# Performance work log

Hardware: AMD Instinct MI355X
Metric: run time of the kernel (lower is better)

The kernel has to match this reference:

```python
import jax, jax.numpy as jnp
import numpy as np

B, T, C, UNITS = 64, 1000, 320, 320


def _lstm_scan(x_tbc, m_tb, W, U, b):
    """Masked LSTM over leading time axis.
    x_tbc: [T,B,C], m_tb: [T,B] bool. Keras gate order i,f,c(g),o.
    Masked steps carry (h,c) through unchanged and emit the carried h,
    matching Keras masking semantics. Returns (ys [T,B,U], h_T [B,U]).
    """
    units = U.shape[0]
    h0 = jnp.zeros((x_tbc.shape[1], units), x_tbc.dtype)

    def step(carry, inp):
        h, c = carry
        xt, mt = inp
        z = xt @ W + h @ U + b                      # [B, 4U]
        i, f, g, o = jnp.split(z, 4, axis=-1)
        i = jax.nn.sigmoid(i)
        f = jax.nn.sigmoid(f)
        g = jnp.tanh(g)
        o = jax.nn.sigmoid(o)
        c_new = f * c + i * g
        h_new = o * jnp.tanh(c_new)
        mt = mt[:, None]
        h = jnp.where(mt, h_new, h)
        c = jnp.where(mt, c_new, c)
        return (h, c), h

    (hT, cT), ys = jax.lax.scan(step, (h0, h0), (x_tbc, m_tb))
    return ys, hT


def setup_inputs() -> dict:
    key = jax.random.key(0)
    ks = jax.random.split(key, 8)
    inputs = jax.random.normal(ks[0], (B, T, C), dtype=jnp.float32)
    # padding mask: variable sequence lengths in [T//2, T]
    seq_len = jax.random.randint(ks[1], (B,), T // 2, T + 1)
    mask = (jnp.arange(T)[None, :] < seq_len[:, None])  # [B, T] bool
    s_in = 1.0 / np.sqrt(C)
    s_rec = 1.0 / np.sqrt(UNITS)
    W_fwd = jax.random.normal(ks[2], (C, 4 * UNITS), jnp.float32) * s_in
    U_fwd = jax.random.normal(ks[3], (UNITS, 4 * UNITS), jnp.float32) * s_rec
    b_fwd = jnp.zeros((4 * UNITS,), jnp.float32).at[UNITS:2 * UNITS].set(1.0)  # unit forget bias
    W_bwd = jax.random.normal(ks[4], (C, 4 * UNITS), jnp.float32) * s_in
    U_bwd = jax.random.normal(ks[5], (UNITS, 4 * UNITS), jnp.float32) * s_rec
    b_bwd = jnp.zeros((4 * UNITS,), jnp.float32).at[UNITS:2 * UNITS].set(1.0)
    return {"inputs": inputs, "mask": mask, "W_fwd": W_fwd, "U_fwd": U_fwd,
            "b_fwd": b_fwd, "W_bwd": W_bwd, "U_bwd": U_bwd, "b_bwd": b_bwd}


def reference(inputs, mask, W_fwd, U_fwd, b_fwd, W_bwd, U_bwd, b_bwd):
    x = jnp.transpose(inputs, (1, 0, 2))   # [T,B,C]
    m = jnp.transpose(mask, (1, 0))        # [T,B]
    # forward direction
    ys_f, h_f = _lstm_scan(x, m, W_fwd, U_fwd, b_fwd)
    # backward direction: go_backwards reverses time; Bidirectional flips output back
    ys_b, h_b = _lstm_scan(x[::-1], m[::-1], W_bwd, U_bwd, b_bwd)
    ys_b = ys_b[::-1]
    sequence_output = jnp.transpose(jnp.concatenate([ys_f, ys_b], axis=-1), (1, 0, 2))  # [B,T,2U]
    state_output = jnp.concatenate([h_f, h_b], axis=-1)  # [B,2U]
    return sequence_output, state_output
```

## Files before the change

### kernel.cpp

```cpp
#include <hip/hip_runtime.h>
#include <hip/hip_bf16.h>
#include <stdint.h>


#define Bx 64
#define Tx 1000
#define Cx 320
#define NSLICE 20
#define UPW 16

typedef __attribute__((ext_vector_type(8))) short short8;
typedef __attribute__((ext_vector_type(4))) short short4v;
typedef __attribute__((ext_vector_type(4))) float f32x4;

__device__ inline unsigned short f2bf(float f) {
  unsigned x = __builtin_bit_cast(unsigned, f);
  x += 0x7fffu + ((x >> 16) & 1u);
  return (unsigned short)(x >> 16);
}
__device__ inline float bf2f(unsigned short u) {
  unsigned x = ((unsigned)u) << 16;
  return __builtin_bit_cast(float, x);
}

#define OFF_MB   0ull
#define OFF_BAR  8192ull
#define OFF_HB   16384ull
#define OFF_XB   0ull
#define OFF_WT   40960000ull
#define OFF_BP   42598400ull
#define OFF_ZX   42608640ull

__global__ __launch_bounds__(256) void k_prep_x(const float* __restrict__ X,
                                                unsigned short* __restrict__ Xb) {
  int i4 = blockIdx.x * 256 + threadIdx.x;
  if (i4 >= Bx * Tx * Cx / 4) return;
  int idx = i4 * 4;
  int b = idx / (Tx * Cx);
  int rem = idx - b * (Tx * Cx);
  int t = rem / Cx;
  int c = rem - t * Cx;
  float4 v = *(const float4*)(X + idx);
  short4v o;
  o[0] = (short)f2bf(v.x); o[1] = (short)f2bf(v.y);
  o[2] = (short)f2bf(v.z); o[3] = (short)f2bf(v.w);
  *(short4v*)(Xb + (size_t)(t * Bx + b) * Cx + c) = o;
}

__global__ __launch_bounds__(256) void k_prep_w(const float* __restrict__ Wf,
                                                const float* __restrict__ Wb,
                                                const float* __restrict__ bfv,
                                                const float* __restrict__ bbv,
                                                unsigned short* __restrict__ Wt,
                                                float* __restrict__ biasp) {
  int gid = blockIdx.x * 256 + threadIdx.x;
  if (gid < 2 * 1280 * 320) {
    int dir = gid / (1280 * 320);
    int rem = gid - dir * 1280 * 320;
    int n = rem / 320;
    int k = rem - n * 320;
    int u = n >> 2, g = n & 3;
    const float* W = dir ? Wb : Wf;
    Wt[gid] = f2bf(W[k * 1280 + g * 320 + u]);
  }
  if (gid < 2 * 1280) {
    int dir = gid / 1280, n = gid - dir * 1280;
    int u = n >> 2, g = n & 3;
    const float* bsrc = dir ? bbv : bfv;
    biasp[gid] = bsrc[g * 320 + u];
  }
}

__global__ __launch_bounds__(256) void k_prep_mask(const void* __restrict__ maskp,
                                                   unsigned long long* __restrict__ mask2) {
  int t = blockIdx.x * 256 + threadIdx.x;
  if (t >= Tx) return;
  const unsigned* mw = (const unsigned*)maskp;
  const bool mbyte = (mw[0] == 0x01010101u);
  unsigned long long wv = 0ull;
  if (mbyte) {
    const unsigned char* m8 = (const unsigned char*)maskp;
#pragma unroll 8
    for (int b = 0; b < Bx; b++)
      wv |= (unsigned long long)(m8[b * Tx + t] & 1) << b;
  } else {
    const int* m32 = (const int*)maskp;
#pragma unroll 8
    for (int b = 0; b < Bx; b++)
      wv |= (unsigned long long)(m32[b * Tx + t] & 1) << b;
  }
  mask2[t] = wv;
}

__global__ __launch_bounds__(256) void k_gemm(const unsigned short* __restrict__ A,
                                              const unsigned short* __restrict__ Bt,
                                              const float* __restrict__ biasp,
                                              unsigned short* __restrict__ Czx) {
  int bid = blockIdx.x;
  int dir = bid / 5000;
  int r = bid - dir * 5000;
  int tm = r / 10, tn = r - (r / 10) * 10;
  long m0 = (long)tm * 128;
  int n0 = tn * 128;
  const unsigned short* Bd = Bt + (size_t)dir * 1280 * 320;
  const float* bias = biasp + dir * 1280;

  __shared__ __align__(16) unsigned short As[128 * 64];
  __shared__ __align__(16) unsigned short Bs[128 * 64];

  int tid = threadIdx.x;
  int wave = tid >> 6, lane = tid & 63;
  int l15 = lane & 15, l4 = lane >> 4;

  f32x4 acc[2][8];
#pragma unroll
  for (int i = 0; i < 2; i++)
#pragma unroll
    for (int j = 0; j < 8; j++) acc[i][j] = (f32x4){0.f, 0.f, 0.f, 0.f};

  for (int k0 = 0; k0 < 320; k0 += 64) {
    __syncthreads();
#pragma unroll
    for (int it = 0; it < 4; it++) {
      int idx = it * 256 + tid;
      int rr = idx >> 3, cc = idx & 7;
      const unsigned short* ga = A + (size_t)(m0 + rr) * 320 + k0 + cc * 8;
      unsigned short* la = As + (size_t)(it * 256 + wave * 64) * 8;
      __builtin_amdgcn_global_load_lds(
          (const __attribute__((address_space(1))) void*)ga,
          (__attribute__((address_space(3))) void*)la, 16, 0, 0);
      const unsigned short* gb = Bd + (size_t)(n0 + rr) * 320 + k0 + cc * 8;
      unsigned short* lb = Bs + (size_t)(it * 256 + wave * 64) * 8;
      __builtin_amdgcn_global_load_lds(
          (const __attribute__((address_space(1))) void*)gb,
          (__attribute__((address_space(3))) void*)lb, 16, 0, 0);
    }
    __syncthreads();
#pragma unroll
    for (int kk = 0; kk < 2; kk++) {
      short8 af[2], bf8[8];
#pragma unroll
      for (int mf = 0; mf < 2; mf++)
        af[mf] = *(const short8*)(As + (wave * 32 + mf * 16 + l15) * 64 + kk * 32 + l4 * 8);
#pragma unroll
      for (int nf = 0; nf < 8; nf++)
        bf8[nf] = *(const short8*)(Bs + (nf * 16 + l15) * 64 + kk * 32 + l4 * 8);
#pragma unroll
      for (int mf = 0; mf < 2; mf++)
#pragma unroll
        for (int nf = 0; nf < 8; nf++)
          acc[mf][nf] = __builtin_amdgcn_mfma_f32_16x16x32_bf16(af[mf], bf8[nf], acc[mf][nf], 0, 0, 0);
    }
  }
#pragma unroll
  for (int mf = 0; mf < 2; mf++) {
#pragma unroll
    for (int nf = 0; nf < 8; nf++) {
      int col = n0 + nf * 16 + l15;
      float bv = bias[col];
      int slice = col >> 6, i64v = col & 63;
      size_t sbase = ((size_t)(dir * NSLICE + slice)) * Tx * 4096;
#pragma unroll
      for (int i = 0; i < 4; i++) {
        long m = m0 + wave * 32 + mf * 16 + l4 * 4 + i;
        long t = m >> 6;
        int b = (int)(m & 63);
        Czx[sbase + (size_t)t * 4096 + b * 64 + i64v] = f2bf(acc[mf][nf][i] + bv);
      }
    }
  }
}

__global__ __launch_bounds__(256, 1) void k_lstm(const unsigned short* __restrict__ Zx,
                                                 const float* __restrict__ Uf,
                                                 const float* __restrict__ Ub,
                                                 const unsigned long long* __restrict__ mask2,
                                                 unsigned short* __restrict__ hbuf,
                                                 float* __restrict__ out,
                                                 unsigned* __restrict__ bar) {
  const int w = blockIdx.x;
  const int dir = w / NSLICE;
  const int slice = w - dir * NSLICE;
  const int u0 = slice * UPW;
  const int tid = threadIdx.x;
  const int wave = tid >> 6, lane = tid & 63;
  const int l15 = lane & 15, l4 = lane >> 4;

  const float* U = dir ? Ub : Uf;
  short8 bfrag[4][10];
#pragma unroll
  for (int nf = 0; nf < 4; nf++) {
    int ncol = nf * 16 + l15;
    int colU = (ncol & 3) * 320 + u0 + (ncol >> 2);
#pragma unroll
    for (int kt = 0; kt < 10; kt++) {
      short8 v;
#pragma unroll
      for (int j = 0; j < 8; j++)
        v[j] = (short)f2bf(U[(size_t)(kt * 32 + l4 * 8 + j) * 1280 + colU]);
      bfrag[nf][kt] = v;
    }
  }

  const int pb = tid >> 2;
  const int uq = tid & 3;
  const int arow = wave * 16 + l15;
  float c0 = 0.f, c1 = 0.f, c2 = 0.f, c3 = 0.f;
  float h0 = 0.f, h1 = 0.f, h2 = 0.f, h3 = 0.f;

  __shared__ float zsh[64][68];

  unsigned* slots = bar + dir * NSLICE * 16;
  const unsigned short* zbase = Zx + ((size_t)(dir * NSLICE + slice)) * Tx * 4096;

  int t = dir ? (Tx - 1) : 0;
  short8 zv0 = *(const short8*)(zbase + (size_t)t * 4096 + pb * 64 + uq * 16);
  short8 zv1 = *(const short8*)(zbase + (size_t)t * 4096 + pb * 64 + uq * 16 + 8);
  unsigned long long mwrd = mask2[t];

  for (int s = 0;; ++s) {
    t = dir ? (Tx - 1 - s) : s;
    float4 zr0, zr1, zr2, zr3;
    if (s > 0) {
      if (tid < NSLICE) {
        while (__hip_atomic_load(&slots[tid * 16], __ATOMIC_RELAXED,
                                 __HIP_MEMORY_SCOPE_AGENT) < (unsigned)s)
          __builtin_amdgcn_s_sleep(1);
      }
      __syncthreads();

      const unsigned short* hr = hbuf + ((size_t)((s & 1) * 2 + dir)) * Bx * 320;
      const unsigned short* hp = hr + arow * 320 + l4 * 8;
      short8 afr[10];
#pragma unroll
      for (int kt = 0; kt < 10; kt++) {
        union { unsigned long long q[2]; short8 v; } u;
        u.q[0] = __hip_atomic_load((const unsigned long long*)(hp + kt * 32),
                                   __ATOMIC_RELAXED, __HIP_MEMORY_SCOPE_AGENT);
        u.q[1] = __hip_atomic_load((const unsigned long long*)(hp + kt * 32 + 4),
                                   __ATOMIC_RELAXED, __HIP_MEMORY_SCOPE_AGENT);
        afr[kt] = u.v;
      }
#pragma unroll
      for (int nf = 0; nf < 4; nf++) {
        f32x4 a0 = {0.f, 0.f, 0.f, 0.f}, a1 = {0.f, 0.f, 0.f, 0.f};
#pragma unroll
        for (int k2 = 0; k2 < 5; k2++) {
          a0 = __builtin_amdgcn_mfma_f32_16x16x32_bf16(afr[2 * k2], bfrag[nf][2 * k2], a0, 0, 0, 0);
          a1 = __builtin_amdgcn_mfma_f32_16x16x32_bf16(afr[2 * k2 + 1], bfrag[nf][2 * k2 + 1], a1, 0, 0, 0);
        }
        int rr = wave * 16 + l4 * 4;
        zsh[rr + 0][nf * 16 + l15] = a0[0] + a1[0];
        zsh[rr + 1][nf * 16 + l15] = a0[1] + a1[1];
        zsh[rr + 2][nf * 16 + l15] = a0[2] + a1[2];
        zsh[rr + 3][nf * 16 + l15] = a0[3] + a1[3];
      }
      __syncthreads();
      zr0 = *(const float4*)&zsh[pb][uq * 16 + 0];
      zr1 = *(const float4*)&zsh[pb][uq * 16 + 4];
      zr2 = *(const float4*)&zsh[pb][uq * 16 + 8];
      zr3 = *(const float4*)&zsh[pb][uq * 16 + 12];
    } else {
      zr0 = zr1 = zr2 = zr3 = make_float4(0.f, 0.f, 0.f, 0.f);
    }

    int mv = (int)((mwrd >> pb) & 1ull);
#define GATES(CC, HH, Z0, Z1, Z2, Z3, ZR)                              \
    {                                                                  \
      float zi = bf2f((unsigned short)(Z0)) + (ZR).x;                  \
      float zf = bf2f((unsigned short)(Z1)) + (ZR).y;                  \
      float zg = bf2f((unsigned short)(Z2)) + (ZR).z;                  \
      float zo = bf2f((unsigned short)(Z3)) + (ZR).w;                  \
      float ig = 1.f / (1.f + __expf(-zi));                            \
      float fg = 1.f / (1.f + __expf(-zf));                            \
      float gg = 2.f / (1.f + __expf(-2.f * zg)) - 1.f;                \
      float og = 1.f / (1.f + __expf(-zo));                            \
      float cn = fg * (CC) + ig * gg;                                  \
      float hn = og * (2.f / (1.f + __expf(-2.f * cn)) - 1.f);         \
      if (mv) { (CC) = cn; (HH) = hn; }                                \
    }
    GATES(c0, h0, zv0[0], zv0[1], zv0[2], zv0[3], zr0)
    GATES(c1, h1, zv0[4], zv0[5], zv0[6], zv0[7], zr1)
    GATES(c2, h2, zv1[0], zv1[1], zv1[2], zv1[3], zr2)
    GATES(c3, h3, zv1[4], zv1[5], zv1[6], zv1[7], zr3)
#undef GATES

    unsigned short* hw = hbuf + ((size_t)(((s + 1) & 1) * 2 + dir)) * Bx * 320;
    unsigned long long hv =
        (unsigned long long)f2bf(h0) | ((unsigned long long)f2bf(h1) << 16) |
        ((unsigned long long)f2bf(h2) << 32) | ((unsigned long long)f2bf(h3) << 48);
    __hip_atomic_store((unsigned long long*)(hw + pb * 320 + u0 + uq * 4), hv,
                       __ATOMIC_RELAXED, __HIP_MEMORY_SCOPE_AGENT);

    __syncthreads();
    if (tid == 0 && s < Tx - 1)
      __hip_atomic_store(&slots[slice * 16], (unsigned)(s + 1), __ATOMIC_RELEASE,
                         __HIP_MEMORY_SCOPE_AGENT);

    union { float f[4]; unsigned long long q[2]; } ou;
    ou.f[0] = h0; ou.f[1] = h1; ou.f[2] = h2; ou.f[3] = h3;
    unsigned long long* op = (unsigned long long*)(out +
        ((size_t)pb * Tx + t) * 640 + dir * 320 + u0 + uq * 4);
    __hip_atomic_store(op, ou.q[0], __ATOMIC_RELAXED, __HIP_MEMORY_SCOPE_AGENT);
    __hip_atomic_store(op + 1, ou.q[1], __ATOMIC_RELAXED, __HIP_MEMORY_SCOPE_AGENT);
    if (s == Tx - 1) {
      unsigned long long* fp = (unsigned long long*)(out + 40960000ull +
          (size_t)pb * 640 + dir * 320 + u0 + uq * 4);
      __hip_atomic_store(fp, ou.q[0], __ATOMIC_RELAXED, __HIP_MEMORY_SCOPE_AGENT);
      __hip_atomic_store(fp + 1, ou.q[1], __ATOMIC_RELAXED, __HIP_MEMORY_SCOPE_AGENT);
      break;
    }

    int tn = dir ? (Tx - 2 - s) : (s + 1);
    zv0 = *(const short8*)(zbase + (size_t)tn * 4096 + pb * 64 + uq * 16);
    zv1 = *(const short8*)(zbase + (size_t)tn * 4096 + pb * 64 + uq * 16 + 8);
    mwrd = mask2[tn];
  }
}

extern "C" void kernel_launch(void* const* d_in, const int* in_sizes, int n_in,
                              void* d_out, int out_size, void* d_ws, size_t ws_size,
                              hipStream_t stream) {
  const float* X = (const float*)d_in[0];
  const void* Mk = d_in[1];
  const float* Wf = (const float*)d_in[2];
  const float* Uf = (const float*)d_in[3];
  const float* bfv = (const float*)d_in[4];
  const float* Wb = (const float*)d_in[5];
  const float* Ub = (const float*)d_in[6];
  const float* bbv = (const float*)d_in[7];

  char* ws = (char*)d_ws;
  unsigned short* Xb = (unsigned short*)(ws + OFF_XB);
  unsigned short* Wt = (unsigned short*)(ws + OFF_WT);
  float* bp = (float*)(ws + OFF_BP);
  unsigned short* Zx = (unsigned short*)(ws + OFF_ZX);
  unsigned long long* mask2 = (unsigned long long*)(ws + OFF_MB);
  unsigned short* hbuf = (unsigned short*)(ws + OFF_HB);
  unsigned* bar = (unsigned*)(ws + OFF_BAR);

  k_prep_x<<<dim3(20000), dim3(256), 0, stream>>>(X, Xb);
  k_prep_w<<<dim3(3200), dim3(256), 0, stream>>>(Wf, Wb, bfv, bbv, Wt, bp);
  k_gemm<<<dim3(10000), dim3(256), 0, stream>>>(Xb, Wt, bp, Zx);
  hipMemsetAsync(ws + OFF_BAR, 0, 2560, stream);
  k_prep_mask<<<dim3(4), dim3(256), 0, stream>>>(Mk, mask2);
  k_lstm<<<dim3(2 * NSLICE), dim3(256), 0, stream>>>(Zx, Uf, Ub, mask2, hbuf,
                                                     (float*)d_out, bar);
}
```

Baseline: 5.669 ms.

## Replace slot-counter barrier with sentinel-flagged h ring buffer polling

The per-step cross-block barrier is removed: one thread per slice no longer spins on a counter, and there is no __syncthreads, flag store or release store per step. Instead each thread polls its own hidden-state words in a 4-slot ring buffer until they differ from an all-ones sentinel. Each block resets the slot two steps ahead to the sentinel, and the loads for the next step are issued early, right after the output stores. This aims to cut per-step synchronisation latency on the serial recurrence. In exchange it relies on relaxed ordering between the data stores and the sentinel resets, adds a 20-register poll buffer per thread, and needs a memset of the ring to 0xFF before launch.

```diff
diff --git a/kernel.cpp b/kernel.cpp
--- a/kernel.cpp
+++ b/kernel.cpp
@@ -8,6 +8,7 @@
 #define Cx 320
 #define NSLICE 20
 #define UPW 16
+#define SENT 0xFFFFFFFFFFFFFFFFull
 
 typedef __attribute__((ext_vector_type(8))) short short8;
 typedef __attribute__((ext_vector_type(4))) short short4v;
@@ -24,7 +25,6 @@
 }
 
 #define OFF_MB   0ull
-#define OFF_BAR  8192ull
 #define OFF_HB   16384ull
 #define OFF_XB   0ull
 #define OFF_WT   40960000ull
@@ -175,9 +175,8 @@
                                                  const float* __restrict__ Uf,
                                                  const float* __restrict__ Ub,
                                                  const unsigned long long* __restrict__ mask2,
-                                                 unsigned short* __restrict__ hbuf,
-                                                 float* __restrict__ out,
-                                                 unsigned* __restrict__ bar) {
+                                                 unsigned short* __restrict__ hring,
+                                                 float* __restrict__ out) {
   const int w = blockIdx.x;
   const int dir = w / NSLICE;
   const int slice = w - dir * NSLICE;
@@ -210,35 +209,38 @@
 
   __shared__ float zsh[64][68];
 
-  unsigned* slots = bar + dir * NSLICE * 16;
   const unsigned short* zbase = Zx + ((size_t)(dir * NSLICE + slice)) * Tx * 4096;
+#define HR(SL) (hring + ((size_t)((SL) * 2 + dir)) * Bx * 320)
 
   int t = dir ? (Tx - 1) : 0;
   short8 zv0 = *(const short8*)(zbase + (size_t)t * 4096 + pb * 64 + uq * 16);
   short8 zv1 = *(const short8*)(zbase + (size_t)t * 4096 + pb * 64 + uq * 16 + 8);
   unsigned long long mwrd = mask2[t];
 
+  unsigned long long q[20];
+  const unsigned long long* pollp = nullptr;
+
   for (int s = 0;; ++s) {
     t = dir ? (Tx - 1 - s) : s;
     float4 zr0, zr1, zr2, zr3;
     if (s > 0) {
-      if (tid < NSLICE) {
-        while (__hip_atomic_load(&slots[tid * 16], __ATOMIC_RELAXED,
-                                 __HIP_MEMORY_SCOPE_AGENT) < (unsigned)s)
-          __builtin_amdgcn_s_sleep(1);
+      for (;;) {
+        bool any = false;
+#pragma unroll
+        for (int i = 0; i < 20; i++) any |= (q[i] == SENT);
+        if (!any) break;
+#pragma unroll
+        for (int i = 0; i < 20; i++)
+          if (q[i] == SENT)
+            q[i] = __hip_atomic_load(pollp + (i >> 1) * 8 + (i & 1),
+                                     __ATOMIC_RELAXED, __HIP_MEMORY_SCOPE_AGENT);
       }
-      __syncthreads();
-
-      const unsigned short* hr = hbuf + ((size_t)((s & 1) * 2 + dir)) * Bx * 320;
-      const unsigned short* hp = hr + arow * 320 + l4 * 8;
       short8 afr[10];
 #pragma unroll
       for (int kt = 0; kt < 10; kt++) {
-        union { unsigned long long q[2]; short8 v; } u;
-        u.q[0] = __hip_atomic_load((const unsigned long long*)(hp + kt * 32),
-                                   __ATOMIC_RELAXED, __HIP_MEMORY_SCOPE_AGENT);
-        u.q[1] = __hip_atomic_load((const unsigned long long*)(hp + kt * 32 + 4),
-                                   __ATOMIC_RELAXED, __HIP_MEMORY_SCOPE_AGENT);
+        union { unsigned long long qq[2]; short8 v; } u;
+        u.qq[0] = q[2 * kt];
+        u.qq[1] = q[2 * kt + 1];
         afr[kt] = u.v;
       }
 #pragma unroll
@@ -285,37 +287,44 @@
     GATES(c3, h3, zv1[4], zv1[5], zv1[6], zv1[7], zr3)
 #undef GATES
 
-    unsigned short* hw = hbuf + ((size_t)(((s + 1) & 1) * 2 + dir)) * Bx * 320;
-    unsigned long long hv =
-        (unsigned long long)f2bf(h0) | ((unsigned long long)f2bf(h1) << 16) |
-        ((unsigned long long)f2bf(h2) << 32) | ((unsigned long long)f2bf(h3) << 48);
-    __hip_atomic_store((unsigned long long*)(hw + pb * 320 + u0 + uq * 4), hv,
-                       __ATOMIC_RELAXED, __HIP_MEMORY_SCOPE_AGENT);
-
-    __syncthreads();
-    if (tid == 0 && s < Tx - 1)
-      __hip_atomic_store(&slots[slice * 16], (unsigned)(s + 1), __ATOMIC_RELEASE,
-                         __HIP_MEMORY_SCOPE_AGENT);
-
-    union { float f[4]; unsigned long long q[2]; } ou;
+    union { float f[4]; unsigned long long qq[2]; } ou;
     ou.f[0] = h0; ou.f[1] = h1; ou.f[2] = h2; ou.f[3] = h3;
+
+    if (s < Tx - 1) {
+      unsigned long long hv =
+          (unsigned long long)f2bf(h0) | ((unsigned long long)f2bf(h1) << 16) |
+          ((unsigned long long)f2bf(h2) << 32) | ((unsigned long long)f2bf(h3) << 48);
+      __hip_atomic_store((unsigned long long*)(HR(s & 3) + pb * 320 + u0 + uq * 4),
+                         hv, __ATOMIC_RELAXED, __HIP_MEMORY_SCOPE_AGENT);
+    }
+
     unsigned long long* op = (unsigned long long*)(out +
         ((size_t)pb * Tx + t) * 640 + dir * 320 + u0 + uq * 4);
-    __hip_atomic_store(op, ou.q[0], __ATOMIC_RELAXED, __HIP_MEMORY_SCOPE_AGENT);
-    __hip_atomic_store(op + 1, ou.q[1], __ATOMIC_RELAXED, __HIP_MEMORY_SCOPE_AGENT);
+    __hip_atomic_store(op, ou.qq[0], __ATOMIC_RELAXED, __HIP_MEMORY_SCOPE_AGENT);
+    __hip_atomic_store(op + 1, ou.qq[1], __ATOMIC_RELAXED, __HIP_MEMORY_SCOPE_AGENT);
     if (s == Tx - 1) {
       unsigned long long* fp = (unsigned long long*)(out + 40960000ull +
           (size_t)pb * 640 + dir * 320 + u0 + uq * 4);
-      __hip_atomic_store(fp, ou.q[0], __ATOMIC_RELAXED, __HIP_MEMORY_SCOPE_AGENT);
-      __hip_atomic_store(fp + 1, ou.q[1], __ATOMIC_RELAXED, __HIP_MEMORY_SCOPE_AGENT);
+      __hip_atomic_store(fp, ou.qq[0], __ATOMIC_RELAXED, __HIP_MEMORY_SCOPE_AGENT);
+      __hip_atomic_store(fp + 1, ou.qq[1], __ATOMIC_RELAXED, __HIP_MEMORY_SCOPE_AGENT);
       break;
     }
+
+    __hip_atomic_store((unsigned long long*)(HR((s + 2) & 3) + pb * 320 + u0 + uq * 4),
+                       SENT, __ATOMIC_RELAXED, __HIP_MEMORY_SCOPE_AGENT);
 
     int tn = dir ? (Tx - 2 - s) : (s + 1);
     zv0 = *(const short8*)(zbase + (size_t)tn * 4096 + pb * 64 + uq * 16);
     zv1 = *(const short8*)(zbase + (size_t)tn * 4096 + pb * 64 + uq * 16 + 8);
     mwrd = mask2[tn];
-  }
+
+    pollp = (const unsigned long long*)(HR(s & 3) + arow * 320 + l4 * 8);
+#pragma unroll
+    for (int i = 0; i < 20; i++)
+      q[i] = __hip_atomic_load(pollp + (i >> 1) * 8 + (i & 1),
+                               __ATOMIC_RELAXED, __HIP_MEMORY_SCOPE_AGENT);
+  }
+#undef HR
 }
 
 extern "C" void kernel_launch(void* const* d_in, const int* in_sizes, int n_in,
@@ -336,14 +345,13 @@
   float* bp = (float*)(ws + OFF_BP);
   unsigned short* Zx = (unsigned short*)(ws + OFF_ZX);
   unsigned long long* mask2 = (unsigned long long*)(ws + OFF_MB);
-  unsigned short* hbuf = (unsigned short*)(ws + OFF_HB);
-  unsigned* bar = (unsigned*)(ws + OFF_BAR);
+  unsigned short* hring = (unsigned short*)(ws + OFF_HB);
 
   k_prep_x<<<dim3(20000), dim3(256), 0, stream>>>(X, Xb);
   k_prep_w<<<dim3(3200), dim3(256), 0, stream>>>(Wf, Wb, bfv, bbv, Wt, bp);
   k_gemm<<<dim3(10000), dim3(256), 0, stream>>>(Xb, Wt, bp, Zx);
-  hipMemsetAsync(ws + OFF_BAR, 0, 2560, stream);
+  hipMemsetAsync(ws + OFF_HB, 0xFF, 327680, stream);
   k_prep_mask<<<dim3(4), dim3(256), 0, stream>>>(Mk, mask2);
-  k_lstm<<<dim3(2 * NSLICE), dim3(256), 0, stream>>>(Zx, Uf, Ub, mask2, hbuf,
-                                                     (float*)d_out, bar);
-}
+  k_lstm<<<dim3(2 * NSLICE), dim3(256), 0, stream>>>(Zx, Uf, Ub, mask2, hring,
+                                                     (float*)d_out);
+}
```

Result: faster. 5.295 ms (median of 2 runs) (-6.6%).
